# Optimization experiments

Hardware: AMD Instinct MI355X
Metric: run time of the kernel (lower is better)

Reference implementation:

```python
import jax, jax.numpy as jnp
import numpy as np

N_MFS = 2
N_FEATURES = 12
OUTPUT_DIM = 8
BATCH = 4096
N_RULES = N_MFS ** N_FEATURES  # 4096


def _rule_indices(n_features, n_mfs):
    r = np.arange(n_mfs ** n_features)
    # mixed-radix digits: indices[rule, feat] = (rule // n_mfs**feat) % n_mfs
    return np.stack([(r // (n_mfs ** f)) % n_mfs for f in range(n_features)], axis=1).astype(np.int32)


def setup_inputs() -> dict:
    key = jax.random.key(0)
    ks = jax.random.split(key, 6)
    x = jax.random.normal(ks[0], (BATCH, N_FEATURES), dtype=jnp.float32)
    center_base = jax.random.uniform(ks[1], (N_FEATURES, 1), minval=-1.0, maxval=0.0, dtype=jnp.float32)
    center_delta_raw = jax.random.normal(ks[2], (N_FEATURES, N_MFS - 1), dtype=jnp.float32) * 0.5
    width_raw = jax.random.normal(ks[3], (N_FEATURES, N_MFS), dtype=jnp.float32) * 0.5
    fan = N_RULES * N_FEATURES + OUTPUT_DIM
    limit = float(np.sqrt(6.0 / fan))
    consequent_p = jax.random.uniform(ks[4], (N_RULES, N_FEATURES, OUTPUT_DIM), minval=-limit, maxval=limit, dtype=jnp.float32)
    consequent_r = jnp.zeros((N_RULES, OUTPUT_DIM), dtype=jnp.float32)
    rule_mf_indices = jnp.asarray(_rule_indices(N_FEATURES, N_MFS))
    return {"x": x, "center_base": center_base, "center_delta_raw": center_delta_raw,
            "width_raw": width_raw, "consequent_p": consequent_p, "consequent_r": consequent_r,
            "rule_mf_indices": rule_mf_indices}


def reference(x, center_base, center_delta_raw, width_raw, consequent_p, consequent_r, rule_mf_indices):
    # ordered centers: base + cumsum(softplus(delta) + 1e-3)
    gaps = jax.nn.softplus(center_delta_raw) + 1e-3          # (F, M-1)
    offsets = jnp.cumsum(gaps, axis=1)
    centers = jnp.concatenate([center_base, center_base + offsets], axis=1)  # (F, M)
    widths = jax.nn.softplus(width_raw) + 1e-3                # (F, M)

    # Gaussian memberships: (B, F, M)
    d = x[:, :, None] - centers[None, :, :]
    memberships = jnp.exp(-jnp.square(d) / (2.0 * jnp.square(widths)[None, :, :]))

    # rule firing: product over features of gathered memberships (loop over small fixed F)
    firing = jnp.ones((x.shape[0], rule_mf_indices.shape[0]), dtype=x.dtype)  # (B, R)
    for f in range(memberships.shape[1]):
        firing = firing * memberships[:, f, :][:, rule_mf_indices[:, f]]
    firing_norm = firing / (jnp.sum(firing, axis=1, keepdims=True) + 1e-8)

    # per-rule linear consequents: (B, R, O)
    rule_outputs = jnp.einsum('bf,rfo->bro', x, consequent_p) + consequent_r[None, :, :]
    # weighted reduce over rules: (B, O)
    output = jnp.einsum('br,bro->bo', firing_norm, rule_outputs)
    return output
```

## Files before the change

### kernel.cpp

```cpp
#include <hip/hip_runtime.h>
#include <math.h>

#define NF 12
#define NB 4096
#define NR 4096
#define NO 8

typedef float f32x4v __attribute__((ext_vector_type(4)));
typedef short bf16x8 __attribute__((ext_vector_type(8)));
typedef unsigned int uint32x4 __attribute__((ext_vector_type(4)));

#define PT2_BYTES (128 * 8 * 512 * 2)
#define PARAMS_OFF PT2_BYTES
#define PT_ELEMS (112 * 4096)

__device__ __forceinline__ float softplus_f(float v) {
    return fmaxf(v, 0.0f) + log1pf(__expf(-fabsf(v)));
}
__device__ __forceinline__ unsigned short f2bf(float f) {
    unsigned u = __float_as_uint(f);
    u += 0x7FFFu + ((u >> 16) & 1u);
    return (unsigned short)(u >> 16);
}
__device__ __forceinline__ unsigned cvt_pk_bf16(float a, float b) {
    unsigned r;
    asm("v_cvt_pk_bf16_f32 %0, %1, %2" : "=v"(r) : "v"(a), "v"(b));
    return r;
}

__device__ __forceinline__ void build_afrag(f32x4v lo0, f32x4v lo1, float hv,
                                            bf16x8& ah, bf16x8& al) {
    float v0 = lo0[0]*hv, v1 = lo0[1]*hv, v2 = lo0[2]*hv, v3 = lo0[3]*hv;
    float v4 = lo1[0]*hv, v5 = lo1[1]*hv, v6 = lo1[2]*hv, v7 = lo1[3]*hv;
    unsigned h0 = cvt_pk_bf16(v0, v1), h1 = cvt_pk_bf16(v2, v3);
    unsigned h2 = cvt_pk_bf16(v4, v5), h3 = cvt_pk_bf16(v6, v7);
    float e0 = v0 - __uint_as_float(h0 << 16), e1 = v1 - __uint_as_float(h0 & 0xFFFF0000u);
    float e2 = v2 - __uint_as_float(h1 << 16), e3 = v3 - __uint_as_float(h1 & 0xFFFF0000u);
    float e4 = v4 - __uint_as_float(h2 << 16), e5 = v5 - __uint_as_float(h2 & 0xFFFF0000u);
    float e6 = v6 - __uint_as_float(h3 << 16), e7 = v7 - __uint_as_float(h3 & 0xFFFF0000u);
    unsigned q0 = cvt_pk_bf16(e0, e1), q1 = cvt_pk_bf16(e2, e3);
    unsigned q2 = cvt_pk_bf16(e4, e5), q3 = cvt_pk_bf16(e6, e7);
    union { uint32x4 u; bf16x8 v; } A, B;
    A.u = (uint32x4){h0, h1, h2, h3};
    B.u = (uint32x4){q0, q1, q2, q3};
    ah = A.v; al = B.v;
}

__global__ __launch_bounds__(512) void anfis_prep2(
    const float* __restrict__ cp, const float* __restrict__ cr,
    const float* __restrict__ center_base, const float* __restrict__ cdr,
    const float* __restrict__ wr,
    unsigned short* __restrict__ PT2, float* __restrict__ params,
    float* __restrict__ out_zero)
{
    __shared__ float s_cp[32 * 97];
    __shared__ float s_cr[32 * 8];
    const int kt = blockIdx.x;
    const int tid = threadIdx.x;

    if (kt < 64) out_zero[(size_t)kt * 512 + tid] = 0.0f;

    {
        const float4* cp4 = (const float4*)(cp + (size_t)kt * 32 * 96);
        for (int i = tid; i < 768; i += 512) {
            float4 v = cp4[i];
            int r = i / 24, c4 = i - r * 24;
            float* d = &s_cp[r * 97 + c4 * 4];
            d[0] = v.x; d[1] = v.y; d[2] = v.z; d[3] = v.w;
        }
        if (tid < 64) {
            float4 v = ((const float4*)(cr + (size_t)kt * 32 * 8))[tid];
            float* d = &s_cr[tid * 4];
            d[0] = v.x; d[1] = v.y; d[2] = v.z; d[3] = v.w;
        }
    }
    __syncthreads();

    const int g = tid >> 7, col = (tid >> 3) & 15, e = tid & 7;
    const int rr = g * 8 + e;
    #pragma unroll
    for (int j = 0; j < 8; ++j) {
        int n = j * 16 + col;
        float v = 0.f;
        if (n < 96) v = s_cp[rr * 97 + n];
        else if (n < 104) v = s_cr[rr * 8 + (n - 96)];
        PT2[(size_t)(kt * 8 + j) * 512 + tid] = f2bf(v);
    }

    if (kt == 0 && tid < NF) {
        float c0 = center_base[tid];
        float gap = softplus_f(cdr[tid]) + 1e-3f;
        float w0 = softplus_f(wr[tid * 2 + 0]) + 1e-3f;
        float w1 = softplus_f(wr[tid * 2 + 1]) + 1e-3f;
        params[tid * 4 + 0] = c0;
        params[tid * 4 + 1] = c0 + gap;
        params[tid * 4 + 2] = -0.5f / (w0 * w0);
        params[tid * 4 + 3] = -0.5f / (w1 * w1);
    }
}

__global__ __launch_bounds__(512, 4) void anfis_main4(
    const float* __restrict__ x,
    const unsigned short* __restrict__ PT2,
    const float* __restrict__ params,
    float* __restrict__ out,
    const int ktPer)
{
    __shared__ float s_mf[64 * 24];
    __shared__ float s_prod[64 * 8];
    __shared__ float s_rcp[64];
    __shared__ float s_x[64 * 12];
    __shared__ float s_low[64 * 36];
    __shared__ float s_high[64 * 36];
    __shared__ __align__(16) unsigned char s_B[2 * 16384];

    const int tid = threadIdx.x;
    const int mt = blockIdx.x & 63;
    const int ks = blockIdx.x >> 6;
    const int b0 = mt * 64;
    const int kt0 = ks * ktPer;
    const int nCh = ktPer >> 1;
    const int nHiPer = ktPer >> 3;

    if (tid < 384) {
        int row = tid / 6, fp = tid - row * 6;
        float pr = 1.f;
        #pragma unroll
        for (int h = 0; h < 2; ++h) {
            int f = fp + h * 6;
            float xv = x[(size_t)(b0 + row) * NF + f];
            s_x[row * 12 + f] = xv;
            float4 pm = *(const float4*)&params[f * 4];
            float d0 = xv - pm.x, d1 = xv - pm.y;
            float m0 = __expf(d0 * d0 * pm.z);
            float m1 = __expf(d1 * d1 * pm.w);
            s_mf[row * 24 + f * 2 + 0] = m0;
            s_mf[row * 24 + f * 2 + 1] = m1;
            pr *= (m0 + m1);
        }
        s_prod[row * 8 + fp] = pr;
    }
    __syncthreads();
    if (tid < 64) {
        float S = 1.f;
        #pragma unroll
        for (int i = 0; i < 6; ++i) S *= s_prod[tid * 8 + i];
        s_rcp[tid] = 1.0f / (S + 1e-8f);
    }
    __syncthreads();

    {
        int row = tid >> 3, w8 = tid & 7;
        const float* mr = &s_mf[row * 24];
        #pragma unroll
        for (int i = 0; i < 4; ++i) {
            int ee = w8 * 4 + i;
            float p = 1.f;
            #pragma unroll
            for (int f = 0; f < 5; ++f) p *= mr[f * 2 + ((ee >> f) & 1)];
            s_low[row * 36 + ee] = p;
        }
        float rc = s_rcp[row];
        for (int i = 0; i < nHiPer; ++i) {
            int t = w8 * nHiPer + i;
            int ktg = kt0 + t;
            float p = rc;
            #pragma unroll
            for (int ff = 0; ff < 7; ++ff) p *= mr[(5 + ff) * 2 + ((ktg >> ff) & 1)];
            s_high[row * 36 + t] = p;
        }
    }
    __syncthreads();

    const int w = tid >> 6, l = tid & 63;
    const int rg = w >> 1, cg = w & 1;
    const int col = l & 15, g = l >> 4;
    const int rowA = rg * 16 + col;

    f32x4v lo0 = *(const f32x4v*)&s_low[rowA * 36 + g * 8];
    f32x4v lo1 = *(const f32x4v*)&s_low[rowA * 36 + g * 8 + 4];
    const float* hptr = &s_high[rowA * 36];

    f32x4v acc[4];
    #pragma unroll
    for (int jj = 0; jj < 4; ++jj) acc[jj] = (f32x4v){0.f, 0.f, 0.f, 0.f};

    const unsigned char* ptBase = (const unsigned char*)PT2;

    #define STAGE(c, buf) do {                                                        \
        const unsigned char* gb = ptBase + ((size_t)(kt0 + 2 * (c)) << 13);           \
        unsigned char* lb = &s_B[(buf) * 16384];                                      \
        __builtin_amdgcn_global_load_lds(                                             \
            (const __attribute__((address_space(1))) void*)(gb + w * 1024 + l * 16),  \
            (__attribute__((address_space(3))) void*)(lb + w * 1024), 16, 0, 0);      \
        __builtin_amdgcn_global_load_lds(                                             \
            (const __attribute__((address_space(1))) void*)(gb + (8 + w) * 1024 + l * 16), \
            (__attribute__((address_space(3))) void*)(lb + (8 + w) * 1024), 16, 0, 0);\
    } while (0)

    STAGE(0, 0);
    __syncthreads();

    for (int c = 0; c < nCh; ++c) {
        const int cur = c & 1;
        if (c + 1 < nCh) STAGE(c + 1, cur ^ 1);
        #pragma unroll
        for (int kt2 = 0; kt2 < 2; ++kt2) {
            const unsigned char* fp8 = &s_B[cur * 16384 + kt2 * 8192 + cg * 4096 + l * 16];
            bf16x8 fr0 = *(const bf16x8*)(fp8);
            bf16x8 fr1 = *(const bf16x8*)(fp8 + 1024);
            bf16x8 fr2 = *(const bf16x8*)(fp8 + 2048);
            bf16x8 fr3 = *(const bf16x8*)(fp8 + 3072);
            float hv = hptr[c * 2 + kt2];
            bf16x8 ah, al;
            build_afrag(lo0, lo1, hv, ah, al);
            acc[0] = __builtin_amdgcn_mfma_f32_16x16x32_bf16(ah, fr0, acc[0], 0, 0, 0);
            acc[0] = __builtin_amdgcn_mfma_f32_16x16x32_bf16(al, fr0, acc[0], 0, 0, 0);
            acc[1] = __builtin_amdgcn_mfma_f32_16x16x32_bf16(ah, fr1, acc[1], 0, 0, 0);
            acc[1] = __builtin_amdgcn_mfma_f32_16x16x32_bf16(al, fr1, acc[1], 0, 0, 0);
            acc[2] = __builtin_amdgcn_mfma_f32_16x16x32_bf16(ah, fr2, acc[2], 0, 0, 0);
            acc[2] = __builtin_amdgcn_mfma_f32_16x16x32_bf16(al, fr2, acc[2], 0, 0, 0);
            acc[3] = __builtin_amdgcn_mfma_f32_16x16x32_bf16(ah, fr3, acc[3], 0, 0, 0);
            acc[3] = __builtin_amdgcn_mfma_f32_16x16x32_bf16(al, fr3, acc[3], 0, 0, 0);
        }
        __syncthreads();
    }
    #undef STAGE

    float* s_acc = (float*)s_B;
    #pragma unroll
    for (int jj = 0; jj < 4; ++jj) {
        if (cg == 0 || jj < 3) {
            int j = cg * 4 + jj;
            #pragma unroll
            for (int q = 0; q < 4; ++q)
                s_acc[(rg * 16 + g * 4 + q) * 116 + j * 16 + col] = acc[jj][q];
        }
    }
    __syncthreads();
    {
        const int row = tid >> 3, o = tid & 7;
        const float* ar = &s_acc[row * 116];
        float t = ar[96 + o];
        #pragma unroll
        for (int f = 0; f < NF; ++f) t = fmaf(s_x[row * 12 + f], ar[f * 8 + o], t);
        atomicAdd(&out[(size_t)(b0 + row) * NO + o], t);
    }
}

__global__ __launch_bounds__(256) void anfis_prep(
    const float* __restrict__ cp, const float* __restrict__ cr,
    unsigned short* __restrict__ PT)
{
    const int n = blockIdx.x;
    const int t = threadIdx.x;
    if (n < 96) {
        #pragma unroll
        for (int i = 0; i < 16; ++i) { int r = i * 256 + t; PT[n * 4096 + r] = f2bf(cp[r * 96 + n]); }
    } else if (n < 104) {
        const int o = n - 96;
        #pragma unroll
        for (int i = 0; i < 16; ++i) { int r = i * 256 + t; PT[n * 4096 + r] = f2bf(cr[r * 8 + o]); }
    } else {
        #pragma unroll
        for (int i = 0; i < 16; ++i) PT[n * 4096 + i * 256 + t] = 0;
    }
}

__global__ __launch_bounds__(512) void anfis_mfma(
    const float* __restrict__ x,
    const float* __restrict__ center_base,
    const float* __restrict__ center_delta_raw,
    const float* __restrict__ width_raw,
    const unsigned short* __restrict__ PT,
    float* __restrict__ out)
{
    __shared__ float s_mem[16 * 26];
    __shared__ float s_low[16 * 36];
    __shared__ float s_high[16 * 132];
    __shared__ float s_red[8 * 16 * 113];

    const int tid = threadIdx.x;
    const int b0 = blockIdx.x * 16;

    if (tid < 16) {
        const int b = b0 + tid;
        float S = 1.0f;
        #pragma unroll
        for (int f = 0; f < NF; ++f) {
            float cb  = center_base[f];
            float gap = softplus_f(center_delta_raw[f]) + 1e-3f;
            float c0 = cb, c1 = cb + gap;
            float w0 = softplus_f(width_raw[f * 2 + 0]) + 1e-3f;
            float w1 = softplus_f(width_raw[f * 2 + 1]) + 1e-3f;
            float xv = x[b * NF + f];
            float d0 = xv - c0, d1 = xv - c1;
            float m0 = __expf(-d0 * d0 / (2.0f * w0 * w0));
            float m1 = __expf(-d1 * d1 / (2.0f * w1 * w1));
            s_mem[tid * 26 + f * 2 + 0] = m0;
            s_mem[tid * 26 + f * 2 + 1] = m1;
            S *= (m0 + m1);
        }
        s_mem[tid * 26 + 24] = 1.0f / (S + 1e-8f);
    }
    __syncthreads();
    if (tid < 256) {
        const int row = tid >> 4, w16 = tid & 15;
        const float* mrow = &s_mem[row * 26];
        #pragma unroll
        for (int e = 2 * w16; e <= 2 * w16 + 1; ++e) {
            float p = 1.0f;
            #pragma unroll
            for (int f = 0; f < 5; ++f) p *= mrow[f * 2 + ((e >> f) & 1)];
            s_low[row * 36 + e] = p;
        }
        float rcp = mrow[24];
        #pragma unroll
        for (int i = 0; i < 8; ++i) {
            int e = w16 + 16 * i;
            float p = rcp;
            #pragma unroll
            for (int ff = 0; ff < 7; ++ff) p *= mrow[(5 + ff) * 2 + ((e >> ff) & 1)];
            s_high[row * 132 + e] = p;
        }
    }
    __syncthreads();

    const int w = tid >> 6;
    const int l = tid & 63;
    const int col = l & 15;
    const int g   = l >> 4;

    f32x4v lo0 = *(const f32x4v*)&s_low[col * 36 + g * 8];
    f32x4v lo1 = *(const f32x4v*)&s_low[col * 36 + g * 8 + 4];
    f32x4v hq0 = *(const f32x4v*)&s_high[col * 132 + w * 16 + 0];
    f32x4v hq1 = *(const f32x4v*)&s_high[col * 132 + w * 16 + 4];
    f32x4v hq2 = *(const f32x4v*)&s_high[col * 132 + w * 16 + 8];
    f32x4v hq3 = *(const f32x4v*)&s_high[col * 132 + w * 16 + 12];

    const unsigned short* pB = PT + (size_t)col * 4096 + g * 8 + w * 512;

    f32x4v acc[7];
    #pragma unroll
    for (int j = 0; j < 7; ++j) acc[j] = (f32x4v){0.f, 0.f, 0.f, 0.f};

    bf16x8 bf[2][7];
    #pragma unroll
    for (int j = 0; j < 7; ++j) bf[0][j] = *(const bf16x8*)(pB + j * 65536 + 0 * 32);
    #pragma unroll
    for (int j = 0; j < 7; ++j) bf[1][j] = *(const bf16x8*)(pB + j * 65536 + 1 * 32);

    #pragma unroll
    for (int s = 0; s < 16; ++s) {
        const float hv = (s < 4) ? hq0[s & 3] : (s < 8) ? hq1[s & 3]
                        : (s < 12) ? hq2[s & 3] : hq3[s & 3];
        bf16x8 ah, al;
        #pragma unroll
        for (int e = 0; e < 8; ++e) {
            float v = ((e < 4) ? lo0[e & 3] : lo1[e & 3]) * hv;
            unsigned short h = f2bf(v);
            float vh = __uint_as_float(((unsigned)h) << 16);
            ah[e] = (short)h;
            al[e] = (short)f2bf(v - vh);
        }
        #pragma unroll
        for (int j = 0; j < 7; ++j) {
            acc[j] = __builtin_amdgcn_mfma_f32_16x16x32_bf16(ah, bf[s & 1][j], acc[j], 0, 0, 0);
            acc[j] = __builtin_amdgcn_mfma_f32_16x16x32_bf16(al, bf[s & 1][j], acc[j], 0, 0, 0);
        }
        if (s + 2 < 16) {
            #pragma unroll
            for (int j = 0; j < 7; ++j)
                bf[s & 1][j] = *(const bf16x8*)(pB + j * 65536 + (s + 2) * 32);
        }
    }

    #pragma unroll
    for (int j = 0; j < 7; ++j)
        #pragma unroll
        for (int q = 0; q < 4; ++q)
            s_red[(w * 16 + g * 4 + q) * 113 + j * 16 + col] = acc[j][q];
    __syncthreads();

    if (tid < 128) {
        const int row = tid >> 3, o = tid & 7;
        float xr[NF];
        #pragma unroll
        for (int f = 0; f < NF; ++f) xr[f] = x[(b0 + row) * NF + f];
        float outv = 0.0f;
        #pragma unroll
        for (int ww = 0; ww < 8; ++ww) {
            const float* ar = &s_red[(ww * 16 + row) * 113];
            float t2 = ar[96 + o];
            #pragma unroll
            for (int f = 0; f < NF; ++f) t2 = fmaf(xr[f], ar[f * 8 + o], t2);
            outv += t2;
        }
        out[(b0 + row) * NO + o] = outv;
    }
}

extern "C" void kernel_launch(void* const* d_in, const int* in_sizes, int n_in,
                              void* d_out, int out_size, void* d_ws, size_t ws_size,
                              hipStream_t stream) {
    const float* x   = (const float*)d_in[0];
    const float* cb  = (const float*)d_in[1];
    const float* cdr = (const float*)d_in[2];
    const float* wr  = (const float*)d_in[3];
    const float* cp  = (const float*)d_in[4];
    const float* cr  = (const float*)d_in[5];
    float* out = (float*)d_out;

    const size_t need_new = (size_t)PARAMS_OFF + 2048;

    if (ws_size >= need_new) {
        const int KS = 8;
        const int ktPer = 128 / KS;
        unsigned short* PT2 = (unsigned short*)d_ws;
        float* params = (float*)((char*)d_ws + PARAMS_OFF);
        anfis_prep2<<<128, 512, 0, stream>>>(cp, cr, cb, cdr, wr, PT2, params, out);
        anfis_main4<<<64 * KS, 512, 0, stream>>>(x, PT2, params, out, ktPer);
    } else if (ws_size >= (size_t)PT_ELEMS * sizeof(unsigned short)) {
        unsigned short* PT = (unsigned short*)d_ws;
        anfis_prep<<<112, 256, 0, stream>>>(cp, cr, PT);
        anfis_mfma<<<NB / 16, 512, 0, stream>>>(x, cb, cdr, wr, PT, out);
    }
}
```

Measured before the change: 22.54 us.

## Issue B-tile prefetch before membership prologue and skip unused MFMA column tile

The main kernel now issues the first two async global-to-LDS loads of the consequent tiles before computing memberships, so the prologue math overlaps with memory latency. x and params are staged through shared memory with a vectorized load. The k-split constants are hardcoded, and block indexing is changed so the 8 k-splits of a row tile are adjacent. Waves with cg==1 skip the fourth MFMA pair, whose results were never stored. The build_afrag arithmetic is rewritten in vector form.

```diff
diff --git a/kernel.cpp b/kernel.cpp
--- a/kernel.cpp
+++ b/kernel.cpp
@@ -12,6 +12,7 @@
 
 #define PT2_BYTES (128 * 8 * 512 * 2)
 #define PARAMS_OFF PT2_BYTES
+#define WS_NEED (PT2_BYTES + 2048)
 #define PT_ELEMS (112 * 4096)
 
 __device__ __forceinline__ float softplus_f(float v) {
@@ -30,16 +31,19 @@
 
 __device__ __forceinline__ void build_afrag(f32x4v lo0, f32x4v lo1, float hv,
                                             bf16x8& ah, bf16x8& al) {
-    float v0 = lo0[0]*hv, v1 = lo0[1]*hv, v2 = lo0[2]*hv, v3 = lo0[3]*hv;
-    float v4 = lo1[0]*hv, v5 = lo1[1]*hv, v6 = lo1[2]*hv, v7 = lo1[3]*hv;
-    unsigned h0 = cvt_pk_bf16(v0, v1), h1 = cvt_pk_bf16(v2, v3);
-    unsigned h2 = cvt_pk_bf16(v4, v5), h3 = cvt_pk_bf16(v6, v7);
-    float e0 = v0 - __uint_as_float(h0 << 16), e1 = v1 - __uint_as_float(h0 & 0xFFFF0000u);
-    float e2 = v2 - __uint_as_float(h1 << 16), e3 = v3 - __uint_as_float(h1 & 0xFFFF0000u);
-    float e4 = v4 - __uint_as_float(h2 << 16), e5 = v5 - __uint_as_float(h2 & 0xFFFF0000u);
-    float e6 = v6 - __uint_as_float(h3 << 16), e7 = v7 - __uint_as_float(h3 & 0xFFFF0000u);
-    unsigned q0 = cvt_pk_bf16(e0, e1), q1 = cvt_pk_bf16(e2, e3);
-    unsigned q2 = cvt_pk_bf16(e4, e5), q3 = cvt_pk_bf16(e6, e7);
+    f32x4v hv4 = {hv, hv, hv, hv};
+    f32x4v va = lo0 * hv4;
+    f32x4v vb = lo1 * hv4;
+    unsigned h0 = cvt_pk_bf16(va[0], va[1]), h1 = cvt_pk_bf16(va[2], va[3]);
+    unsigned h2 = cvt_pk_bf16(vb[0], vb[1]), h3 = cvt_pk_bf16(vb[2], vb[3]);
+    f32x4v hia = { __uint_as_float(h0 << 16), __uint_as_float(h0 & 0xFFFF0000u),
+                   __uint_as_float(h1 << 16), __uint_as_float(h1 & 0xFFFF0000u) };
+    f32x4v hib = { __uint_as_float(h2 << 16), __uint_as_float(h2 & 0xFFFF0000u),
+                   __uint_as_float(h3 << 16), __uint_as_float(h3 & 0xFFFF0000u) };
+    f32x4v ea = va - hia;
+    f32x4v eb = vb - hib;
+    unsigned q0 = cvt_pk_bf16(ea[0], ea[1]), q1 = cvt_pk_bf16(ea[2], ea[3]);
+    unsigned q2 = cvt_pk_bf16(eb[0], eb[1]), q3 = cvt_pk_bf16(eb[2], eb[3]);
     union { uint32x4 u; bf16x8 v; } A, B;
     A.u = (uint32x4){h0, h1, h2, h3};
     B.u = (uint32x4){q0, q1, q2, q3};
@@ -99,13 +103,13 @@
     }
 }
 
-__global__ __launch_bounds__(512, 4) void anfis_main4(
+__global__ __launch_bounds__(512, 4) void anfis_main6(
     const float* __restrict__ x,
     const unsigned short* __restrict__ PT2,
     const float* __restrict__ params,
-    float* __restrict__ out,
-    const int ktPer)
+    float* __restrict__ out)
 {
+    __shared__ float s_params[48];
     __shared__ float s_mf[64 * 24];
     __shared__ float s_prod[64 * 8];
     __shared__ float s_rcp[64];
@@ -115,78 +119,15 @@
     __shared__ __align__(16) unsigned char s_B[2 * 16384];
 
     const int tid = threadIdx.x;
-    const int mt = blockIdx.x & 63;
-    const int ks = blockIdx.x >> 6;
+    const int bid = blockIdx.x;
+    const int ks = bid & 7;
+    const int mt = bid >> 3;
     const int b0 = mt * 64;
-    const int kt0 = ks * ktPer;
-    const int nCh = ktPer >> 1;
-    const int nHiPer = ktPer >> 3;
-
-    if (tid < 384) {
-        int row = tid / 6, fp = tid - row * 6;
-        float pr = 1.f;
-        #pragma unroll
-        for (int h = 0; h < 2; ++h) {
-            int f = fp + h * 6;
-            float xv = x[(size_t)(b0 + row) * NF + f];
-            s_x[row * 12 + f] = xv;
-            float4 pm = *(const float4*)&params[f * 4];
-            float d0 = xv - pm.x, d1 = xv - pm.y;
-            float m0 = __expf(d0 * d0 * pm.z);
-            float m1 = __expf(d1 * d1 * pm.w);
-            s_mf[row * 24 + f * 2 + 0] = m0;
-            s_mf[row * 24 + f * 2 + 1] = m1;
-            pr *= (m0 + m1);
-        }
-        s_prod[row * 8 + fp] = pr;
-    }
-    __syncthreads();
-    if (tid < 64) {
-        float S = 1.f;
-        #pragma unroll
-        for (int i = 0; i < 6; ++i) S *= s_prod[tid * 8 + i];
-        s_rcp[tid] = 1.0f / (S + 1e-8f);
-    }
-    __syncthreads();
-
-    {
-        int row = tid >> 3, w8 = tid & 7;
-        const float* mr = &s_mf[row * 24];
-        #pragma unroll
-        for (int i = 0; i < 4; ++i) {
-            int ee = w8 * 4 + i;
-            float p = 1.f;
-            #pragma unroll
-            for (int f = 0; f < 5; ++f) p *= mr[f * 2 + ((ee >> f) & 1)];
-            s_low[row * 36 + ee] = p;
-        }
-        float rc = s_rcp[row];
-        for (int i = 0; i < nHiPer; ++i) {
-            int t = w8 * nHiPer + i;
-            int ktg = kt0 + t;
-            float p = rc;
-            #pragma unroll
-            for (int ff = 0; ff < 7; ++ff) p *= mr[(5 + ff) * 2 + ((ktg >> ff) & 1)];
-            s_high[row * 36 + t] = p;
-        }
-    }
-    __syncthreads();
+    const int kt0 = ks * 16;
 
     const int w = tid >> 6, l = tid & 63;
-    const int rg = w >> 1, cg = w & 1;
-    const int col = l & 15, g = l >> 4;
-    const int rowA = rg * 16 + col;
-
-    f32x4v lo0 = *(const f32x4v*)&s_low[rowA * 36 + g * 8];
-    f32x4v lo1 = *(const f32x4v*)&s_low[rowA * 36 + g * 8 + 4];
-    const float* hptr = &s_high[rowA * 36];
-
-    f32x4v acc[4];
-    #pragma unroll
-    for (int jj = 0; jj < 4; ++jj) acc[jj] = (f32x4v){0.f, 0.f, 0.f, 0.f};
 
     const unsigned char* ptBase = (const unsigned char*)PT2;
-
     #define STAGE(c, buf) do {                                                        \
         const unsigned char* gb = ptBase + ((size_t)(kt0 + 2 * (c)) << 13);           \
         unsigned char* lb = &s_B[(buf) * 16384];                                      \
@@ -199,18 +140,91 @@
     } while (0)
 
     STAGE(0, 0);
-    __syncthreads();
-
-    for (int c = 0; c < nCh; ++c) {
+    STAGE(1, 1);
+
+    if (tid < 192) {
+        float4 v = ((const float4*)(x + (size_t)b0 * NF))[tid];
+        float* d = &s_x[tid * 4];
+        d[0] = v.x; d[1] = v.y; d[2] = v.z; d[3] = v.w;
+    }
+    if (tid >= 500) {
+        int f = tid - 500;
+        ((float4*)s_params)[f] = ((const float4*)params)[f];
+    }
+    __syncthreads();
+
+    if (tid < 384) {
+        int row = tid / 6, fp = tid - row * 6;
+        float pr = 1.f;
+        #pragma unroll
+        for (int h = 0; h < 2; ++h) {
+            int f = fp + h * 6;
+            float xv = s_x[row * 12 + f];
+            float4 pm = *(const float4*)&s_params[f * 4];
+            float d0 = xv - pm.x, d1 = xv - pm.y;
+            float m0 = __expf(d0 * d0 * pm.z);
+            float m1 = __expf(d1 * d1 * pm.w);
+            s_mf[row * 24 + f * 2 + 0] = m0;
+            s_mf[row * 24 + f * 2 + 1] = m1;
+            pr *= (m0 + m1);
+        }
+        s_prod[row * 8 + fp] = pr;
+    }
+    __syncthreads();
+    if (tid < 64) {
+        float S = 1.f;
+        #pragma unroll
+        for (int i = 0; i < 6; ++i) S *= s_prod[tid * 8 + i];
+        s_rcp[tid] = 1.0f / (S + 1e-8f);
+    }
+    __syncthreads();
+
+    {
+        int row = tid >> 3, w8 = tid & 7;
+        const float* mr = &s_mf[row * 24];
+        #pragma unroll
+        for (int i = 0; i < 4; ++i) {
+            int ee = w8 * 4 + i;
+            float p = 1.f;
+            #pragma unroll
+            for (int f = 0; f < 5; ++f) p *= mr[f * 2 + ((ee >> f) & 1)];
+            s_low[row * 36 + ee] = p;
+        }
+        float rc = s_rcp[row];
+        #pragma unroll
+        for (int i = 0; i < 2; ++i) {
+            int t = w8 * 2 + i;
+            int ktg = kt0 + t;
+            float p = rc;
+            #pragma unroll
+            for (int ff = 0; ff < 7; ++ff) p *= mr[(5 + ff) * 2 + ((ktg >> ff) & 1)];
+            s_high[row * 36 + t] = p;
+        }
+    }
+    __syncthreads();
+
+    const int rg = w >> 1, cg = w & 1;
+    const int col = l & 15, g = l >> 4;
+    const int rowA = rg * 16 + col;
+
+    f32x4v lo0 = *(const f32x4v*)&s_low[rowA * 36 + g * 8];
+    f32x4v lo1 = *(const f32x4v*)&s_low[rowA * 36 + g * 8 + 4];
+    const float* hptr = &s_high[rowA * 36];
+
+    f32x4v acc[4];
+    #pragma unroll
+    for (int jj = 0; jj < 4; ++jj) acc[jj] = (f32x4v){0.f, 0.f, 0.f, 0.f};
+
+    #pragma unroll 1
+    for (int c = 0; c < 8; ++c) {
         const int cur = c & 1;
-        if (c + 1 < nCh) STAGE(c + 1, cur ^ 1);
+        if (c >= 1 && c + 1 < 8) STAGE(c + 1, cur ^ 1);
         #pragma unroll
         for (int kt2 = 0; kt2 < 2; ++kt2) {
             const unsigned char* fp8 = &s_B[cur * 16384 + kt2 * 8192 + cg * 4096 + l * 16];
             bf16x8 fr0 = *(const bf16x8*)(fp8);
             bf16x8 fr1 = *(const bf16x8*)(fp8 + 1024);
             bf16x8 fr2 = *(const bf16x8*)(fp8 + 2048);
-            bf16x8 fr3 = *(const bf16x8*)(fp8 + 3072);
             float hv = hptr[c * 2 + kt2];
             bf16x8 ah, al;
             build_afrag(lo0, lo1, hv, ah, al);
@@ -220,8 +234,11 @@
             acc[1] = __builtin_amdgcn_mfma_f32_16x16x32_bf16(al, fr1, acc[1], 0, 0, 0);
             acc[2] = __builtin_amdgcn_mfma_f32_16x16x32_bf16(ah, fr2, acc[2], 0, 0, 0);
             acc[2] = __builtin_amdgcn_mfma_f32_16x16x32_bf16(al, fr2, acc[2], 0, 0, 0);
-            acc[3] = __builtin_amdgcn_mfma_f32_16x16x32_bf16(ah, fr3, acc[3], 0, 0, 0);
-            acc[3] = __builtin_amdgcn_mfma_f32_16x16x32_bf16(al, fr3, acc[3], 0, 0, 0);
+            if (cg == 0) {
+                bf16x8 fr3 = *(const bf16x8*)(fp8 + 3072);
+                acc[3] = __builtin_amdgcn_mfma_f32_16x16x32_bf16(ah, fr3, acc[3], 0, 0, 0);
+                acc[3] = __builtin_amdgcn_mfma_f32_16x16x32_bf16(al, fr3, acc[3], 0, 0, 0);
+            }
         }
         __syncthreads();
     }
@@ -411,15 +428,11 @@
     const float* cr  = (const float*)d_in[5];
     float* out = (float*)d_out;
 
-    const size_t need_new = (size_t)PARAMS_OFF + 2048;
-
-    if (ws_size >= need_new) {
-        const int KS = 8;
-        const int ktPer = 128 / KS;
+    if (ws_size >= (size_t)WS_NEED) {
         unsigned short* PT2 = (unsigned short*)d_ws;
         float* params = (float*)((char*)d_ws + PARAMS_OFF);
         anfis_prep2<<<128, 512, 0, stream>>>(cp, cr, cb, cdr, wr, PT2, params, out);
-        anfis_main4<<<64 * KS, 512, 0, stream>>>(x, PT2, params, out, ktPer);
+        anfis_main6<<<512, 512, 0, stream>>>(x, PT2, params, out);
     } else if (ws_size >= (size_t)PT_ELEMS * sizeof(unsigned short)) {
         unsigned short* PT = (unsigned short*)d_ws;
         anfis_prep<<<112, 256, 0, stream>>>(cp, cr, PT);
```

New measurement: 22.35 us. No clear change (-0.9%).
